# Performance work log

Measured on AMD Instinct MI355X. Metric: run time of the kernel, lower is better.

The kernel has to match this reference:

```python
import jax, jax.numpy as jnp
import numpy as np

NUM_HEAD = 16
FEAT_DIM = 1024
HEAD_DIM = FEAT_DIM // NUM_HEAD  # 64
MAX_SEQ_LEN = 2048
BATCH = 2


def setup_inputs() -> dict:
    key = jax.random.key(0)
    ks = jax.random.split(key, 6)
    x = jax.random.normal(ks[0], (BATCH, MAX_SEQ_LEN, FEAT_DIM), dtype=jnp.float32)
    # xavier_uniform: limit = sqrt(6/(fan_in+fan_out)); torch Linear weight is [out, in]
    def xavier(k, out_f, in_f):
        lim = float(np.sqrt(6.0 / (in_f + out_f)))
        return jax.random.uniform(k, (out_f, in_f), dtype=jnp.float32, minval=-lim, maxval=lim)
    W1 = xavier(ks[1], HEAD_DIM, HEAD_DIM)          # attn_mlp[0].weight
    b1 = jnp.zeros((HEAD_DIM,), dtype=jnp.float32)
    W2 = xavier(ks[2], MAX_SEQ_LEN, HEAD_DIM)       # attn_mlp[2].weight
    b2 = jnp.zeros((MAX_SEQ_LEN,), dtype=jnp.float32)
    Wv = xavier(ks[3], FEAT_DIM, FEAT_DIM)          # value_linear.weight (no bias)
    Wo = xavier(ks[4], FEAT_DIM, FEAT_DIM)          # output_linear.weight (no bias)
    return {"x": x, "W1": W1, "b1": b1, "W2": W2, "b2": b2, "Wv": Wv, "Wo": Wo}


def _split_head(t):
    b, n, _ = t.shape
    return t.reshape(b, n, NUM_HEAD, HEAD_DIM).transpose(0, 2, 1, 3)  # [b,h,n,d]


def reference(x, W1, b1, W2, b2, Wv, Wo):
    # value projection (dropout is identity in eval / p=0)
    value = x @ Wv.T                                   # [b,n,F]
    vh = _split_head(value)                            # [b,h,n,d]
    xh = _split_head(x)                                # [b,h,n,d]
    # per-head MLP -> dense attention logits [b,h,n,max_seq_len]
    hid = jax.nn.relu(jnp.einsum('bhnd,ed->bhne', xh, W1) + b1)
    logits = jnp.einsum('bhne,me->bhnm', hid, W2) + b2
    attn = jax.nn.softmax(logits, axis=-1)             # [b,h,n,m]
    out_h = jnp.einsum('bhnm,bhmd->bhnd', attn, vh)    # m == seq_len
    b_, h_, n_, d_ = out_h.shape
    out = out_h.transpose(0, 2, 1, 3).reshape(b_, n_, FEAT_DIM)
    return out @ Wo.T
```

## Files before the change

kernel.cpp:

```cpp
#include <hip/hip_runtime.h>
#include <hip/hip_bf16.h>
#include <math.h>
#include <stdint.h>


typedef __attribute__((ext_vector_type(8))) short bf16x8;
typedef __attribute__((ext_vector_type(4))) float f32x4;
typedef __attribute__((ext_vector_type(16))) float f32x16;

#define LOG2E 1.4426950408889634f

__device__ __forceinline__ unsigned short f2bf(float f) {
  union { float f; unsigned u; } v; v.f = f;
  unsigned r = v.u + 0x7FFFu + ((v.u >> 16) & 1u);
  return (unsigned short)(r >> 16);
}

__global__ __launch_bounds__(256) void prep_all(const float* __restrict__ x,
                                                const float* __restrict__ Wv,
                                                const float* __restrict__ Wo,
                                                const float* __restrict__ W2,
                                                const float* __restrict__ W1,
                                                const float* __restrict__ b2,
                                                unsigned short* __restrict__ xb,
                                                unsigned short* __restrict__ wvb,
                                                unsigned short* __restrict__ wob,
                                                unsigned short* __restrict__ w2b,
                                                unsigned short* __restrict__ w1b,
                                                float* __restrict__ eb2f,
                                                unsigned short* __restrict__ ebb) {
  int bid = blockIdx.x;
  if (bid == 2048) {
    int i = threadIdx.x;
#pragma unroll
    for (int t = 0; t < 8; ++t) {
      int k = i * 8 + t;
      float e = __expf(b2[k]);
      eb2f[k] = e;
      ebb[k] = f2bf(e);
    }
    return;
  }
  int stride = 2048 * 256;
  for (int q = bid * 256 + threadIdx.x; q < 1606656; q += stride) {
    const float* s; unsigned short* d; int o;
    if (q < 1048576)      { s = x;  d = xb;  o = q; }
    else {
      int q2 = q - 1048576;
      if (q2 < 262144)      { s = Wv; d = wvb; o = q2; }
      else if (q2 < 524288) { s = Wo; d = wob; o = q2 - 262144; }
      else if (q2 < 557056) { s = W2; d = w2b; o = q2 - 524288; }
      else                  { s = W1; d = w1b; o = q2 - 557056; }
    }
    float4 v = *(const float4*)(s + (size_t)o * 4);
    uint2 u;
    u.x = (unsigned)f2bf(v.x) | ((unsigned)f2bf(v.y) << 16);
    u.y = (unsigned)f2bf(v.z) | ((unsigned)f2bf(v.w) << 16);
    *(uint2*)(d + (size_t)o * 4) = u;
  }
}

__device__ __forceinline__ void stage64(const char* g, size_t ldbytes, char* lds,
                                        int w, int lane) {
#pragma unroll
  for (int t = 0; t < 2; ++t) {
    int row  = w * 16 + t * 8 + (lane >> 3);
    int csrc = (lane & 7) ^ (lane >> 3);
    const char* src = g + (size_t)row * ldbytes + (csrc << 4);
    char* dst = lds + ((w * 2 + t) << 10);
    __builtin_amdgcn_global_load_lds((const __attribute__((address_space(1))) void*)src,
                                     (__attribute__((address_space(3))) void*)dst,
                                     16, 0, 0);
  }
}

__device__ __forceinline__ void stage8(const char* g, size_t ldbytes, char* lds_,
                                       int w, int lane) {
  int row  = w * 8 + (lane >> 3);
  int csrc = (lane & 7) ^ (lane >> 3);
  const char* src = g + (size_t)row * ldbytes + (csrc << 4);
  char* dst = lds_ + (w << 10);
  __builtin_amdgcn_global_load_lds((const __attribute__((address_space(1))) void*)src,
                                   (__attribute__((address_space(3))) void*)dst,
                                   16, 0, 0);
}

__device__ __forceinline__ bf16x8 rdfrag32(const char* lds, int row, int chunk) {
  int c = chunk ^ (row & 7);
  return *(const bf16x8*)(lds + row * 128 + (c << 4));
}

__device__ __forceinline__ f32x16 loadb16(const float* p) {
  f32x16 r;
#pragma unroll
  for (int qd = 0; qd < 4; ++qd) {
    float4 v = *(const float4*)(p + qd * 8);
    r[qd * 4 + 0] = v.x; r[qd * 4 + 1] = v.y; r[qd * 4 + 2] = v.z; r[qd * 4 + 3] = v.w;
  }
  return r;
}

__device__ __forceinline__ bf16x8 pk_swap(float r0, float r1, float r2, float r3,
                                          float r4, float r5, float r6, float r7) {
  unsigned a, b, c, d;
  asm("v_cvt_pk_bf16_f32 %0, %1, %2" : "=v"(a) : "v"(r0), "v"(r1));
  asm("v_cvt_pk_bf16_f32 %0, %1, %2" : "=v"(b) : "v"(r4), "v"(r5));
  asm("v_cvt_pk_bf16_f32 %0, %1, %2" : "=v"(c) : "v"(r2), "v"(r3));
  asm("v_cvt_pk_bf16_f32 %0, %1, %2" : "=v"(d) : "v"(r6), "v"(r7));
  asm("v_permlane32_swap_b32 %0, %1" : "+v"(a), "+v"(b));
  asm("v_permlane32_swap_b32 %0, %1" : "+v"(c), "+v"(d));
  union { unsigned u[4]; bf16x8 v; } r;
  r.u[0] = a; r.u[1] = c; r.u[2] = b; r.u[3] = d;
  return r.v;
}

template<int MODE>
__global__ __launch_bounds__(256) void gemm128(const unsigned short* __restrict__ A,
                                               const unsigned short* __restrict__ B,
                                               void* __restrict__ C,
                                               const float* __restrict__ eb2f, int K) {
  __shared__ __attribute__((aligned(16))) char As[2][16384];
  __shared__ __attribute__((aligned(16))) char Bs[2][16384];
  int tid = threadIdx.x, w = tid >> 6, lane = tid & 63;
  int l31 = lane & 31, hi = lane >> 5;
  int wr = w >> 1, wc = w & 1;
  int bm = blockIdx.x, bn = blockIdx.y;
  const char* Ab = (const char*)A + (size_t)bm * 128 * (K * 2);
  const char* Bb = (const char*)B + (size_t)bn * 128 * (K * 2);
  size_t ld = (size_t)K * 2;

  f32x16 acc00 = {}, acc01 = {}, acc10 = {}, acc11 = {};
  stage64(Ab, ld, As[0], w, lane);
  stage64(Ab + 64 * ld, ld, As[0] + 8192, w, lane);
  stage64(Bb, ld, Bs[0], w, lane);
  stage64(Bb + 64 * ld, ld, Bs[0] + 8192, w, lane);
  __syncthreads();

  int nst = K >> 6;
  for (int kk = 0; kk < nst; ++kk) {
    int cur = kk & 1;
    if (kk + 1 < nst) {
      const char* An = Ab + (size_t)(kk + 1) * 128;
      const char* Bn = Bb + (size_t)(kk + 1) * 128;
      stage64(An, ld, As[cur ^ 1], w, lane);
      stage64(An + 64 * ld, ld, As[cur ^ 1] + 8192, w, lane);
      stage64(Bn, ld, Bs[cur ^ 1], w, lane);
      stage64(Bn + 64 * ld, ld, Bs[cur ^ 1] + 8192, w, lane);
    }
    __builtin_amdgcn_s_setprio(1);
#pragma unroll
    for (int ks = 0; ks < 4; ++ks) {
      bf16x8 a0 = rdfrag32(As[cur], wr * 64 + l31, ks * 2 + hi);
      bf16x8 a1 = rdfrag32(As[cur], wr * 64 + 32 + l31, ks * 2 + hi);
      bf16x8 b0 = rdfrag32(Bs[cur], wc * 64 + l31, ks * 2 + hi);
      bf16x8 b1 = rdfrag32(Bs[cur], wc * 64 + 32 + l31, ks * 2 + hi);
      acc00 = __builtin_amdgcn_mfma_f32_32x32x16_bf16(a0, b0, acc00, 0, 0, 0);
      acc01 = __builtin_amdgcn_mfma_f32_32x32x16_bf16(a0, b1, acc01, 0, 0, 0);
      acc10 = __builtin_amdgcn_mfma_f32_32x32x16_bf16(a1, b0, acc10, 0, 0, 0);
      acc11 = __builtin_amdgcn_mfma_f32_32x32x16_bf16(a1, b1, acc11, 0, 0, 0);
    }
    __builtin_amdgcn_s_setprio(0);
    __syncthreads();
  }

  if (MODE == 0) {
    unsigned short* vt = (unsigned short*)C;
#pragma unroll
    for (int i = 0; i < 2; ++i) {
      int rowb = bm * 128 + wr * 64 + i * 32;
#pragma unroll
      for (int qd = 0; qd < 4; ++qd) {
        int m0 = rowb + qd * 8 + hi * 4;
        float4 e4 = *(const float4*)(eb2f + (m0 & 2047));
        int bb = m0 >> 11, n = m0 & 2047;
#pragma unroll
        for (int j = 0; j < 2; ++j) {
          int h = bn * 2 + wc, d = j * 32 + l31;
          f32x16 a = (i == 0) ? (j == 0 ? acc00 : acc01) : (j == 0 ? acc10 : acc11);
          int r0 = qd * 4;
          uint2 u;
          u.x = (unsigned)f2bf(a[r0] * e4.x) | ((unsigned)f2bf(a[r0 + 1] * e4.y) << 16);
          u.y = (unsigned)f2bf(a[r0 + 2] * e4.z) | ((unsigned)f2bf(a[r0 + 3] * e4.w) << 16);
          *(uint2*)(vt + ((size_t)((bb * 16 + h) * 64 + d)) * 2048 + n) = u;
        }
      }
    }
  } else {
    float* Cf = (float*)C;
    int rb = bm * 128 + wr * 64, cb = bn * 128 + wc * 64;
#pragma unroll
    for (int r = 0; r < 16; ++r) {
      int row = (r & 3) + 8 * (r >> 2) + 4 * hi;
      Cf[(size_t)(rb + row) * 1024 + cb + l31]          = acc00[r];
      Cf[(size_t)(rb + row) * 1024 + cb + 32 + l31]     = acc01[r];
      Cf[(size_t)(rb + 32 + row) * 1024 + cb + l31]     = acc10[r];
      Cf[(size_t)(rb + 32 + row) * 1024 + cb + 32 + l31] = acc11[r];
    }
  }
}

__global__ __launch_bounds__(512, 4) void flash_kernel(const unsigned short* __restrict__ xb,
                                                       const unsigned short* __restrict__ w1b,
                                                       const float* __restrict__ b1,
                                                       const unsigned short* __restrict__ w2b,
                                                       const unsigned short* __restrict__ ebb,
                                                       const unsigned short* __restrict__ vt,
                                                       unsigned short* __restrict__ aout) {
  __shared__ __attribute__((aligned(16))) char lds[65536];
  int tid = threadIdx.x, w = tid >> 6, lane = tid & 63;
  int wq = w & 3, grp = w >> 2;
  int l31 = lane & 31, hi = lane >> 5;
  int f = blockIdx.x;
  int swz = ((f & 7) << 6) | (f >> 3);
  int qt = swz & 15, bh = swz >> 4;
  int b = bh >> 4, h = bh & 15;

  const char* px = (const char*)(xb + ((size_t)(b * 2048 + qt * 128)) * 1024 + h * 64);
  stage8(px, 2048, lds, w, lane);
  stage8(px + (size_t)64 * 2048, 2048, lds + 8192, w, lane);
  stage8((const char*)w1b, 128, lds + 32768, w, lane);
  __syncthreads();

  f32x16 h0 = loadb16(b1 + hi * 4);
  f32x16 h1 = loadb16(b1 + 32 + hi * 4);
  {
    const char* xt = lds + (wq >> 1) * 8192;
    int xr = (wq & 1) * 32 + l31;
#pragma unroll
    for (int ks = 0; ks < 4; ++ks) {
      bf16x8 xf = rdfrag32(xt, xr, ks * 2 + hi);
      bf16x8 wf0 = rdfrag32(lds + 32768, l31, ks * 2 + hi);
      h0 = __builtin_amdgcn_mfma_f32_32x32x16_bf16(wf0, xf, h0, 0, 0, 0);
      bf16x8 wf1 = rdfrag32(lds + 32768, 32 + l31, ks * 2 + hi);
      h1 = __builtin_amdgcn_mfma_f32_32x32x16_bf16(wf1, xf, h1, 0, 0, 0);
    }
  }
#pragma unroll
  for (int i = 0; i < 16; ++i) {
    h0[i] = fmaxf(h0[i], 0.f) * LOG2E;
    h1[i] = fmaxf(h1[i], 0.f) * LOG2E;
  }
  bf16x8 qb[4];
  qb[0] = pk_swap(h0[0], h0[1], h0[2], h0[3], h0[4], h0[5], h0[6], h0[7]);
  qb[1] = pk_swap(h0[8], h0[9], h0[10], h0[11], h0[12], h0[13], h0[14], h0[15]);
  qb[2] = pk_swap(h1[0], h1[1], h1[2], h1[3], h1[4], h1[5], h1[6], h1[7]);
  qb[3] = pk_swap(h1[8], h1[9], h1[10], h1[11], h1[12], h1[13], h1[14], h1[15]);
  __syncthreads();

  const char* vtb = (const char*)vt + (size_t)bh * 64 * 4096;
#pragma unroll
  for (int t = 0; t < 4; ++t) {
    stage8((const char*)w2b + (size_t)t * 8192, 128, lds + t * 8192, w, lane);
    stage8(vtb + (size_t)t * 128, 4096, lds + 32768 + t * 8192, w, lane);
  }
  const f32x16 zro = {};
  f32x16 oA = {}, oB = {}, L = {};
  __syncthreads();

  for (int s = 0; s < 16; ++s) {
    int mt = 2 * s + grp;
    const char* Kc = lds + (mt & 3) * 8192;
    const char* Vc = lds + 32768 + (mt & 3) * 8192;

    bf16x8 ebf0 = *(const bf16x8*)(ebb + mt * 64 + hi * 8);
    bf16x8 ebf1 = *(const bf16x8*)(ebb + mt * 64 + 16 + hi * 8);
    bf16x8 ebf2 = *(const bf16x8*)(ebb + mt * 64 + 32 + hi * 8);
    bf16x8 ebf3 = *(const bf16x8*)(ebb + mt * 64 + 48 + hi * 8);

    f32x16 s0 = zro, s1 = zro;
    __builtin_amdgcn_s_setprio(1);
#pragma unroll
    for (int kt = 0; kt < 4; ++kt) {
      bf16x8 kf0 = rdfrag32(Kc, l31, kt * 2 + hi);
      s0 = __builtin_amdgcn_mfma_f32_32x32x16_bf16(kf0, qb[kt], s0, 0, 0, 0);
      bf16x8 kf1 = rdfrag32(Kc, 32 + l31, kt * 2 + hi);
      s1 = __builtin_amdgcn_mfma_f32_32x32x16_bf16(kf1, qb[kt], s1, 0, 0, 0);
    }
    __builtin_amdgcn_s_setprio(0);
#pragma unroll
    for (int i = 0; i < 16; ++i) {
      float t0, t1;
      asm("v_exp_f32 %0, %1" : "=v"(t0) : "v"(s0[i]));
      asm("v_exp_f32 %0, %1" : "=v"(t1) : "v"(s1[i]));
      s0[i] = t0; s1[i] = t1;
    }
    bf16x8 pa0 = pk_swap(s0[0], s0[1], s0[2], s0[3], s0[4], s0[5], s0[6], s0[7]);
    bf16x8 pa1 = pk_swap(s0[8], s0[9], s0[10], s0[11], s0[12], s0[13], s0[14], s0[15]);
    bf16x8 pa2 = pk_swap(s1[0], s1[1], s1[2], s1[3], s1[4], s1[5], s1[6], s1[7]);
    bf16x8 pa3 = pk_swap(s1[8], s1[9], s1[10], s1[11], s1[12], s1[13], s1[14], s1[15]);
    __builtin_amdgcn_s_setprio(1);
    L = __builtin_amdgcn_mfma_f32_32x32x16_bf16(pa0, ebf0, L, 0, 0, 0);
    L = __builtin_amdgcn_mfma_f32_32x32x16_bf16(pa1, ebf1, L, 0, 0, 0);
    L = __builtin_amdgcn_mfma_f32_32x32x16_bf16(pa2, ebf2, L, 0, 0, 0);
    L = __builtin_amdgcn_mfma_f32_32x32x16_bf16(pa3, ebf3, L, 0, 0, 0);
    {
      bf16x8 vf;
      vf = rdfrag32(Vc, l31, 0 + hi);
      oA = __builtin_amdgcn_mfma_f32_32x32x16_bf16(pa0, vf, oA, 0, 0, 0);
      vf = rdfrag32(Vc, 32 + l31, 0 + hi);
      oB = __builtin_amdgcn_mfma_f32_32x32x16_bf16(pa0, vf, oB, 0, 0, 0);
      vf = rdfrag32(Vc, l31, 2 + hi);
      oA = __builtin_amdgcn_mfma_f32_32x32x16_bf16(pa1, vf, oA, 0, 0, 0);
      vf = rdfrag32(Vc, 32 + l31, 2 + hi);
      oB = __builtin_amdgcn_mfma_f32_32x32x16_bf16(pa1, vf, oB, 0, 0, 0);
      vf = rdfrag32(Vc, l31, 4 + hi);
      oA = __builtin_amdgcn_mfma_f32_32x32x16_bf16(pa2, vf, oA, 0, 0, 0);
      vf = rdfrag32(Vc, 32 + l31, 4 + hi);
      oB = __builtin_amdgcn_mfma_f32_32x32x16_bf16(pa2, vf, oB, 0, 0, 0);
      vf = rdfrag32(Vc, l31, 6 + hi);
      oA = __builtin_amdgcn_mfma_f32_32x32x16_bf16(pa3, vf, oA, 0, 0, 0);
      vf = rdfrag32(Vc, 32 + l31, 6 + hi);
      oB = __builtin_amdgcn_mfma_f32_32x32x16_bf16(pa3, vf, oB, 0, 0, 0);
    }
    __builtin_amdgcn_s_setprio(0);
    __syncthreads();
    if (s < 14) {
      int t0 = 2 * s + 4, t1 = 2 * s + 5;
      stage8((const char*)w2b + (size_t)t0 * 8192, 128, lds + (t0 & 3) * 8192, w, lane);
      stage8(vtb + (size_t)t0 * 128, 4096, lds + 32768 + (t0 & 3) * 8192, w, lane);
      stage8((const char*)w2b + (size_t)t1 * 8192, 128, lds + (t1 & 3) * 8192, w, lane);
      stage8(vtb + (size_t)t1 * 128, 4096, lds + 32768 + (t1 & 3) * 8192, w, lane);
    }
  }

  float* comb = (float*)lds;
  if (grp == 1) {
    float* cb = comb + (wq * 64 + lane) * 52;
#pragma unroll
    for (int i = 0; i < 4; ++i) {
      *(float4*)(cb + i * 4)      = make_float4(oA[i*4], oA[i*4+1], oA[i*4+2], oA[i*4+3]);
      *(float4*)(cb + 16 + i * 4) = make_float4(oB[i*4], oB[i*4+1], oB[i*4+2], oB[i*4+3]);
      *(float4*)(cb + 32 + i * 4) = make_float4(L[i*4],  L[i*4+1],  L[i*4+2],  L[i*4+3]);
    }
  }
  __syncthreads();
  if (grp == 0) {
    float* cb = comb + (wq * 64 + lane) * 52;
#pragma unroll
    for (int i = 0; i < 4; ++i) {
      float4 a = *(const float4*)(cb + i * 4);
      float4 bq = *(const float4*)(cb + 16 + i * 4);
      float4 c = *(const float4*)(cb + 32 + i * 4);
      oA[i*4] += a.x; oA[i*4+1] += a.y; oA[i*4+2] += a.z; oA[i*4+3] += a.w;
      oB[i*4] += bq.x; oB[i*4+1] += bq.y; oB[i*4+2] += bq.z; oB[i*4+3] += bq.w;
      L[i*4] += c.x;  L[i*4+1] += c.y;  L[i*4+2] += c.z;  L[i*4+3] += c.w;
    }
    int nb = qt * 128 + wq * 32;
#pragma unroll
    for (int r = 0; r < 16; ++r) {
      float iv = 1.f / L[r];
      int ql = (r & 3) + 8 * (r >> 2) + 4 * hi;
      size_t off = ((size_t)(b * 2048 + nb + ql)) * 1024 + h * 64 + l31;
      aout[off]      = f2bf(oA[r] * iv);
      aout[off + 32] = f2bf(oB[r] * iv);
    }
  }
}

extern "C" void kernel_launch(void* const* d_in, const int* in_sizes, int n_in,
                              void* d_out, int out_size, void* d_ws, size_t ws_size,
                              hipStream_t stream) {
  (void)in_sizes; (void)n_in; (void)out_size; (void)ws_size;
  const float* x  = (const float*)d_in[0];
  const float* W1 = (const float*)d_in[1];
  const float* b1 = (const float*)d_in[2];
  const float* W2 = (const float*)d_in[3];
  const float* b2 = (const float*)d_in[4];
  const float* Wv = (const float*)d_in[5];
  const float* Wo = (const float*)d_in[6];
  float* out = (float*)d_out;

  char* ws = (char*)d_ws;
  unsigned short* xb   = (unsigned short*)(ws);
  unsigned short* wvb  = (unsigned short*)(ws +  8388608);
  unsigned short* wob  = (unsigned short*)(ws + 10485760);
  unsigned short* w2b  = (unsigned short*)(ws + 12582912);
  unsigned short* w1b  = (unsigned short*)(ws + 12845056);
  float*          eb2f = (float*)         (ws + 12853248);
  unsigned short* ebb  = (unsigned short*)(ws + 12861440);
  unsigned short* vt   = (unsigned short*)(ws + 21233664);
  unsigned short* aout = (unsigned short*)(ws + 29622272);

  prep_all<<<2049, 256, 0, stream>>>(x, Wv, Wo, W2, W1, b2,
                                     xb, wvb, wob, w2b, w1b, eb2f, ebb);

  gemm128<0><<<dim3(32, 8), 256, 0, stream>>>(xb, wvb, (void*)vt, eb2f, 1024);
  flash_kernel<<<512, 512, 0, stream>>>(xb, w1b, b1, w2b, ebb, vt, aout);
  gemm128<1><<<dim3(32, 8), 256, 0, stream>>>(aout, wob, (void*)out, eb2f, 1024);
}
```

Baseline: 98.11 us.

## Fold b2 bias into logits, sum softmax denominator in VALU, use 128x64 GEMM tiles

The b2 bias is now added directly to the logit accumulators, pre-scaled by log2e, instead of being folded in as exp(b2) into V and into an extra MFMA. This removes the four L-accumulating MFMAs per step and the exp(b2) scaling in the V-projection epilogue. The softmax denominator is instead accumulated with scalar adds and reduced across lanes with shuffles at the end, which also shrinks the LDS combine buffer. The GEMMs switch to 128x64 tiles, doubling the grid to 512 blocks for better CU occupancy, at the cost of more A-tile reloads.

```diff
diff --git a/kernel.cpp b/kernel.cpp
--- a/kernel.cpp
+++ b/kernel.cpp
@@ -27,17 +27,14 @@
                                                 unsigned short* __restrict__ wob,
                                                 unsigned short* __restrict__ w2b,
                                                 unsigned short* __restrict__ w1b,
-                                                float* __restrict__ eb2f,
-                                                unsigned short* __restrict__ ebb) {
+                                                float* __restrict__ b2l) {
   int bid = blockIdx.x;
   if (bid == 2048) {
     int i = threadIdx.x;
 #pragma unroll
     for (int t = 0; t < 8; ++t) {
       int k = i * 8 + t;
-      float e = __expf(b2[k]);
-      eb2f[k] = e;
-      ebb[k] = f2bf(e);
+      b2l[k] = b2[k] * LOG2E;
     }
     return;
   }
@@ -115,25 +112,23 @@
 }
 
 template<int MODE>
-__global__ __launch_bounds__(256) void gemm128(const unsigned short* __restrict__ A,
-                                               const unsigned short* __restrict__ B,
-                                               void* __restrict__ C,
-                                               const float* __restrict__ eb2f, int K) {
+__global__ __launch_bounds__(256) void gemm12864(const unsigned short* __restrict__ A,
+                                                 const unsigned short* __restrict__ B,
+                                                 void* __restrict__ C, int K) {
   __shared__ __attribute__((aligned(16))) char As[2][16384];
-  __shared__ __attribute__((aligned(16))) char Bs[2][16384];
+  __shared__ __attribute__((aligned(16))) char Bs[2][8192];
   int tid = threadIdx.x, w = tid >> 6, lane = tid & 63;
   int l31 = lane & 31, hi = lane >> 5;
   int wr = w >> 1, wc = w & 1;
   int bm = blockIdx.x, bn = blockIdx.y;
   const char* Ab = (const char*)A + (size_t)bm * 128 * (K * 2);
-  const char* Bb = (const char*)B + (size_t)bn * 128 * (K * 2);
+  const char* Bb = (const char*)B + (size_t)bn * 64 * (K * 2);
   size_t ld = (size_t)K * 2;
 
-  f32x16 acc00 = {}, acc01 = {}, acc10 = {}, acc11 = {};
+  f32x16 acc0 = {}, acc1 = {};
   stage64(Ab, ld, As[0], w, lane);
   stage64(Ab + 64 * ld, ld, As[0] + 8192, w, lane);
   stage64(Bb, ld, Bs[0], w, lane);
-  stage64(Bb + 64 * ld, ld, Bs[0] + 8192, w, lane);
   __syncthreads();
 
   int nst = K >> 6;
@@ -145,19 +140,15 @@
       stage64(An, ld, As[cur ^ 1], w, lane);
       stage64(An + 64 * ld, ld, As[cur ^ 1] + 8192, w, lane);
       stage64(Bn, ld, Bs[cur ^ 1], w, lane);
-      stage64(Bn + 64 * ld, ld, Bs[cur ^ 1] + 8192, w, lane);
     }
     __builtin_amdgcn_s_setprio(1);
 #pragma unroll
     for (int ks = 0; ks < 4; ++ks) {
       bf16x8 a0 = rdfrag32(As[cur], wr * 64 + l31, ks * 2 + hi);
       bf16x8 a1 = rdfrag32(As[cur], wr * 64 + 32 + l31, ks * 2 + hi);
-      bf16x8 b0 = rdfrag32(Bs[cur], wc * 64 + l31, ks * 2 + hi);
-      bf16x8 b1 = rdfrag32(Bs[cur], wc * 64 + 32 + l31, ks * 2 + hi);
-      acc00 = __builtin_amdgcn_mfma_f32_32x32x16_bf16(a0, b0, acc00, 0, 0, 0);
-      acc01 = __builtin_amdgcn_mfma_f32_32x32x16_bf16(a0, b1, acc01, 0, 0, 0);
-      acc10 = __builtin_amdgcn_mfma_f32_32x32x16_bf16(a1, b0, acc10, 0, 0, 0);
-      acc11 = __builtin_amdgcn_mfma_f32_32x32x16_bf16(a1, b1, acc11, 0, 0, 0);
+      bf16x8 b0 = rdfrag32(Bs[cur], wc * 32 + l31, ks * 2 + hi);
+      acc0 = __builtin_amdgcn_mfma_f32_32x32x16_bf16(a0, b0, acc0, 0, 0, 0);
+      acc1 = __builtin_amdgcn_mfma_f32_32x32x16_bf16(a1, b0, acc1, 0, 0, 0);
     }
     __builtin_amdgcn_s_setprio(0);
     __syncthreads();
@@ -165,36 +156,30 @@
 
   if (MODE == 0) {
     unsigned short* vt = (unsigned short*)C;
+    int d = wc * 32 + l31;
 #pragma unroll
     for (int i = 0; i < 2; ++i) {
+      f32x16 a = i ? acc1 : acc0;
       int rowb = bm * 128 + wr * 64 + i * 32;
 #pragma unroll
       for (int qd = 0; qd < 4; ++qd) {
         int m0 = rowb + qd * 8 + hi * 4;
-        float4 e4 = *(const float4*)(eb2f + (m0 & 2047));
         int bb = m0 >> 11, n = m0 & 2047;
-#pragma unroll
-        for (int j = 0; j < 2; ++j) {
-          int h = bn * 2 + wc, d = j * 32 + l31;
-          f32x16 a = (i == 0) ? (j == 0 ? acc00 : acc01) : (j == 0 ? acc10 : acc11);
-          int r0 = qd * 4;
-          uint2 u;
-          u.x = (unsigned)f2bf(a[r0] * e4.x) | ((unsigned)f2bf(a[r0 + 1] * e4.y) << 16);
-          u.y = (unsigned)f2bf(a[r0 + 2] * e4.z) | ((unsigned)f2bf(a[r0 + 3] * e4.w) << 16);
-          *(uint2*)(vt + ((size_t)((bb * 16 + h) * 64 + d)) * 2048 + n) = u;
-        }
+        int r0 = qd * 4;
+        uint2 u;
+        u.x = (unsigned)f2bf(a[r0]) | ((unsigned)f2bf(a[r0 + 1]) << 16);
+        u.y = (unsigned)f2bf(a[r0 + 2]) | ((unsigned)f2bf(a[r0 + 3]) << 16);
+        *(uint2*)(vt + ((size_t)((bb * 16 + bn) * 64 + d)) * 2048 + n) = u;
       }
     }
   } else {
     float* Cf = (float*)C;
-    int rb = bm * 128 + wr * 64, cb = bn * 128 + wc * 64;
+    int rb = bm * 128 + wr * 64, cb = bn * 64 + wc * 32;
 #pragma unroll
     for (int r = 0; r < 16; ++r) {
       int row = (r & 3) + 8 * (r >> 2) + 4 * hi;
-      Cf[(size_t)(rb + row) * 1024 + cb + l31]          = acc00[r];
-      Cf[(size_t)(rb + row) * 1024 + cb + 32 + l31]     = acc01[r];
-      Cf[(size_t)(rb + 32 + row) * 1024 + cb + l31]     = acc10[r];
-      Cf[(size_t)(rb + 32 + row) * 1024 + cb + 32 + l31] = acc11[r];
+      Cf[(size_t)(rb + row) * 1024 + cb + l31]      = acc0[r];
+      Cf[(size_t)(rb + 32 + row) * 1024 + cb + l31] = acc1[r];
     }
   }
 }
@@ -203,7 +188,7 @@
                                                        const unsigned short* __restrict__ w1b,
                                                        const float* __restrict__ b1,
                                                        const unsigned short* __restrict__ w2b,
-                                                       const unsigned short* __restrict__ ebb,
+                                                       const float* __restrict__ b2l,
                                                        const unsigned short* __restrict__ vt,
                                                        unsigned short* __restrict__ aout) {
   __shared__ __attribute__((aligned(16))) char lds[65536];
@@ -253,8 +238,14 @@
     stage8((const char*)w2b + (size_t)t * 8192, 128, lds + t * 8192, w, lane);
     stage8(vtb + (size_t)t * 128, 4096, lds + 32768 + t * 8192, w, lane);
   }
-  const f32x16 zro = {};
-  f32x16 oA = {}, oB = {}, L = {};
+  f32x4 pre0[4], pre1[4];
+#pragma unroll
+  for (int qd = 0; qd < 4; ++qd) {
+    pre0[qd] = *(const f32x4*)(b2l + grp * 64 + qd * 8 + hi * 4);
+    pre1[qd] = *(const f32x4*)(b2l + grp * 64 + 32 + qd * 8 + hi * 4);
+  }
+  f32x16 oA = {}, oB = {};
+  float lrs0 = 0.f, lrs1 = 0.f, lrs2 = 0.f, lrs3 = 0.f;
   __syncthreads();
 
   for (int s = 0; s < 16; ++s) {
@@ -262,12 +253,15 @@
     const char* Kc = lds + (mt & 3) * 8192;
     const char* Vc = lds + 32768 + (mt & 3) * 8192;
 
-    bf16x8 ebf0 = *(const bf16x8*)(ebb + mt * 64 + hi * 8);
-    bf16x8 ebf1 = *(const bf16x8*)(ebb + mt * 64 + 16 + hi * 8);
-    bf16x8 ebf2 = *(const bf16x8*)(ebb + mt * 64 + 32 + hi * 8);
-    bf16x8 ebf3 = *(const bf16x8*)(ebb + mt * 64 + 48 + hi * 8);
-
-    f32x16 s0 = zro, s1 = zro;
+    f32x16 s0, s1;
+#pragma unroll
+    for (int qd = 0; qd < 4; ++qd) {
+#pragma unroll
+      for (int j = 0; j < 4; ++j) {
+        s0[qd * 4 + j] = pre0[qd][j];
+        s1[qd * 4 + j] = pre1[qd][j];
+      }
+    }
     __builtin_amdgcn_s_setprio(1);
 #pragma unroll
     for (int kt = 0; kt < 4; ++kt) {
@@ -277,22 +271,29 @@
       s1 = __builtin_amdgcn_mfma_f32_32x32x16_bf16(kf1, qb[kt], s1, 0, 0, 0);
     }
     __builtin_amdgcn_s_setprio(0);
+    if (s < 15) {
+#pragma unroll
+      for (int qd = 0; qd < 4; ++qd) {
+        pre0[qd] = *(const f32x4*)(b2l + (mt + 2) * 64 + qd * 8 + hi * 4);
+        pre1[qd] = *(const f32x4*)(b2l + (mt + 2) * 64 + 32 + qd * 8 + hi * 4);
+      }
+    }
 #pragma unroll
     for (int i = 0; i < 16; ++i) {
       float t0, t1;
       asm("v_exp_f32 %0, %1" : "=v"(t0) : "v"(s0[i]));
       asm("v_exp_f32 %0, %1" : "=v"(t1) : "v"(s1[i]));
       s0[i] = t0; s1[i] = t1;
+      if ((i & 3) == 0) { lrs0 += t0; lrs0 += t1; }
+      else if ((i & 3) == 1) { lrs1 += t0; lrs1 += t1; }
+      else if ((i & 3) == 2) { lrs2 += t0; lrs2 += t1; }
+      else { lrs3 += t0; lrs3 += t1; }
     }
     bf16x8 pa0 = pk_swap(s0[0], s0[1], s0[2], s0[3], s0[4], s0[5], s0[6], s0[7]);
     bf16x8 pa1 = pk_swap(s0[8], s0[9], s0[10], s0[11], s0[12], s0[13], s0[14], s0[15]);
     bf16x8 pa2 = pk_swap(s1[0], s1[1], s1[2], s1[3], s1[4], s1[5], s1[6], s1[7]);
     bf16x8 pa3 = pk_swap(s1[8], s1[9], s1[10], s1[11], s1[12], s1[13], s1[14], s1[15]);
     __builtin_amdgcn_s_setprio(1);
-    L = __builtin_amdgcn_mfma_f32_32x32x16_bf16(pa0, ebf0, L, 0, 0, 0);
-    L = __builtin_amdgcn_mfma_f32_32x32x16_bf16(pa1, ebf1, L, 0, 0, 0);
-    L = __builtin_amdgcn_mfma_f32_32x32x16_bf16(pa2, ebf2, L, 0, 0, 0);
-    L = __builtin_amdgcn_mfma_f32_32x32x16_bf16(pa3, ebf3, L, 0, 0, 0);
     {
       bf16x8 vf;
       vf = rdfrag32(Vc, l31, 0 + hi);
@@ -323,36 +324,41 @@
     }
   }
 
+  float lpart = (lrs0 + lrs1) + (lrs2 + lrs3);
   float* comb = (float*)lds;
   if (grp == 1) {
-    float* cb = comb + (wq * 64 + lane) * 52;
+    float* cb = comb + (wq * 64 + lane) * 36;
 #pragma unroll
     for (int i = 0; i < 4; ++i) {
       *(float4*)(cb + i * 4)      = make_float4(oA[i*4], oA[i*4+1], oA[i*4+2], oA[i*4+3]);
       *(float4*)(cb + 16 + i * 4) = make_float4(oB[i*4], oB[i*4+1], oB[i*4+2], oB[i*4+3]);
-      *(float4*)(cb + 32 + i * 4) = make_float4(L[i*4],  L[i*4+1],  L[i*4+2],  L[i*4+3]);
-    }
+    }
+    cb[32] = lpart;
   }
   __syncthreads();
   if (grp == 0) {
-    float* cb = comb + (wq * 64 + lane) * 52;
+    float* cb = comb + (wq * 64 + lane) * 36;
 #pragma unroll
     for (int i = 0; i < 4; ++i) {
       float4 a = *(const float4*)(cb + i * 4);
       float4 bq = *(const float4*)(cb + 16 + i * 4);
-      float4 c = *(const float4*)(cb + 32 + i * 4);
       oA[i*4] += a.x; oA[i*4+1] += a.y; oA[i*4+2] += a.z; oA[i*4+3] += a.w;
       oB[i*4] += bq.x; oB[i*4+1] += bq.y; oB[i*4+2] += bq.z; oB[i*4+3] += bq.w;
-      L[i*4] += c.x;  L[i*4+1] += c.y;  L[i*4+2] += c.z;  L[i*4+3] += c.w;
-    }
+    }
+    float l = lpart + cb[32];
+    l += __shfl_xor(l, 32);
+    float inv = 1.f / l;
+    float iv[16];
+#pragma unroll
+    for (int r = 0; r < 16; ++r)
+      iv[r] = __shfl(inv, (r & 3) + 8 * (r >> 2) + 4 * hi);
     int nb = qt * 128 + wq * 32;
 #pragma unroll
     for (int r = 0; r < 16; ++r) {
-      float iv = 1.f / L[r];
       int ql = (r & 3) + 8 * (r >> 2) + 4 * hi;
       size_t off = ((size_t)(b * 2048 + nb + ql)) * 1024 + h * 64 + l31;
-      aout[off]      = f2bf(oA[r] * iv);
-      aout[off + 32] = f2bf(oB[r] * iv);
+      aout[off]      = f2bf(oA[r] * iv[r]);
+      aout[off + 32] = f2bf(oB[r] * iv[r]);
     }
   }
 }
@@ -376,15 +382,14 @@
   unsigned short* wob  = (unsigned short*)(ws + 10485760);
   unsigned short* w2b  = (unsigned short*)(ws + 12582912);
   unsigned short* w1b  = (unsigned short*)(ws + 12845056);
-  float*          eb2f = (float*)         (ws + 12853248);
-  unsigned short* ebb  = (unsigned short*)(ws + 12861440);
+  float*          b2l  = (float*)         (ws + 12853248);
   unsigned short* vt   = (unsigned short*)(ws + 21233664);
   unsigned short* aout = (unsigned short*)(ws + 29622272);
 
   prep_all<<<2049, 256, 0, stream>>>(x, Wv, Wo, W2, W1, b2,
-                                     xb, wvb, wob, w2b, w1b, eb2f, ebb);
-
-  gemm128<0><<<dim3(32, 8), 256, 0, stream>>>(xb, wvb, (void*)vt, eb2f, 1024);
-  flash_kernel<<<512, 512, 0, stream>>>(xb, w1b, b1, w2b, ebb, vt, aout);
-  gemm128<1><<<dim3(32, 8), 256, 0, stream>>>(aout, wob, (void*)out, eb2f, 1024);
-}
+                                     xb, wvb, wob, w2b, w1b, b2l);
+
+  gemm12864<0><<<dim3(32, 16), 256, 0, stream>>>(xb, wvb, (void*)vt, 1024);
+  flash_kernel<<<512, 512, 0, stream>>>(xb, w1b, b1, w2b, b2l, vt, aout);
+  gemm12864<1><<<dim3(32, 16), 256, 0, stream>>>(aout, wob, (void*)out, 1024);
+}
```

After: 138.1 us. 40.7% more time.
